# Kernel optimization log

Measured on AMD Instinct MI355X. Metric: run time of the kernel, lower is better.

The kernel has to match this reference:

```python
import jax, jax.numpy as jnp
import numpy as np

B, L, D, FF = 4, 4096, 1024, 2048
EPS = 1e-5


def _ln(x, g, b):
    m = jnp.mean(x, axis=-1, keepdims=True)
    v = jnp.var(x, axis=-1, keepdims=True)
    return (x - m) / jnp.sqrt(v + EPS) * g + b


def setup_inputs() -> dict:
    key = jax.random.key(0)
    ks = jax.random.split(key, 9)
    x = jax.random.normal(ks[0], (B, L, D), jnp.float32)
    # phazor init: exp(2j*pi*k/D) * |randn| -> split into re/im float params
    mag = jnp.abs(jax.random.normal(ks[1], (D,), jnp.float32))
    ang = 2.0 * jnp.pi * jnp.arange(D, dtype=jnp.float32) / D
    return dict(
        x=x,
        ln_g=jnp.ones((D,), jnp.float32),
        ln_b=jnp.zeros((D,), jnp.float32),
        fc_w=jax.random.normal(ks[2], (D, D), jnp.float32) * 0.02,
        fc_b=jnp.zeros((D,), jnp.float32),
        w1=jax.random.normal(ks[3], (D, FF), jnp.float32) * 0.02,
        b1=jnp.zeros((FF,), jnp.float32),
        w2=jax.random.normal(ks[4], (FF, D), jnp.float32) * 0.02,
        b2=jnp.zeros((D,), jnp.float32),
        ph_re=mag * jnp.cos(ang),
        ph_im=mag * jnp.sin(ang),
        phi_re=jax.random.normal(ks[5], (D,), jnp.float32),
        phi_im=jax.random.normal(ks[6], (D,), jnp.float32),
        lci_re=jax.random.normal(ks[7], (D,), jnp.float32),
        lci_im=jax.random.normal(ks[8], (D,), jnp.float32),
    )


def _spiral_conv(xn, ph_re, ph_im, phi_re, phi_im, lci_re, lci_im):
    ph = ph_re + 1j * ph_im          # phazor parameter [D]
    phi = phi_re + 1j * phi_im       # phazor_init [D]
    lci = lci_re + 1j * lci_im       # last_conv_init [D]
    a = jnp.abs(ph)
    phz = ph / a * jnp.exp(-a)       # unit direction * decaying magnitude, [D]
    t = jnp.arange(L, dtype=jnp.float32)[:, None]
    prog = jnp.exp(t * jnp.log(phz)[None, :])        # phz**t, [L, D]
    filt = prog * phi[None, :]                       # [L, D]
    filt_fft = jnp.fft.fft(filt, n=2 * L, axis=0)    # [2L, D]
    x_fft = jnp.fft.fft(xn.astype(jnp.complex64), n=2 * L, axis=1)  # [B, 2L, D]
    conv = jnp.fft.ifft(filt_fft[None] * x_fft, axis=1)[:, :L]      # [B, L, D]
    # last_conv is detached in the original (first call uses last_conv_init)
    last = jax.lax.stop_gradient(lci)
    conv = conv + last[None, None, :] * prog[None] * phz[None, None, :]
    return conv.real


def reference(x, ln_g, ln_b, fc_w, fc_b, w1, b1, w2, b2,
              ph_re, ph_im, phi_re, phi_im, lci_re, lci_im):
    xn = _ln(x, ln_g, ln_b)
    c = _spiral_conv(xn, ph_re, ph_im, phi_re, phi_im, lci_re, lci_im)
    y = jax.nn.silu(x @ fc_w + fc_b)
    x2 = c * y + x                  # gated conv + residual (dropout=0 -> identity)
    x3 = _ln(x2, ln_g, ln_b)        # same (shared) LayerNorm instance
    h = jax.nn.silu(x3 @ w1 + b1) @ w2 + b2
    return x2 + h
```

## Files before the change

kernel.cpp:

```cpp
#include <hip/hip_runtime.h>
#include <hip/hip_bf16.h>
#include <hip/hip_fp8.h>
#include <cstdint>
#include <cstddef>

#define B_ 4
#define L_ 4096
#define D_ 1024
#define FF_ 2048
#define ROWS (B_ * L_)
#define EPS_ 1e-5f
#define CG 64
#define CC 64

typedef __attribute__((ext_vector_type(8))) __bf16 bf16x8;
typedef __attribute__((ext_vector_type(4))) float f32x4;
typedef __attribute__((ext_vector_type(4))) unsigned short us4;
typedef __attribute__((ext_vector_type(2))) long l2;

__device__ __forceinline__ float bf2f(unsigned short u) {
  union { unsigned int i; float f; } v; v.i = ((unsigned int)u) << 16; return v.f;
}
__device__ __forceinline__ unsigned short f2bf(float f) {
  union { float f; unsigned int i; } v; v.f = f;
  unsigned int r = v.i + 0x7fffu + ((v.i >> 16) & 1u);
  return (unsigned short)(r >> 16);
}
__device__ __forceinline__ unsigned char f2fp8(float f) {
  __hip_fp8_e4m3 q(f);
  return *reinterpret_cast<unsigned char*>(&q);
}
__device__ __forceinline__ int ph64(int e) {
  return (((e >> 3) & 3) << 4) | (((e >> 5) & 1) << 3) | (e & 7);
}

__global__ __launch_bounds__(256) void transpose_cast(
    const float* __restrict__ in, unsigned short* __restrict__ out, int K, int N) {
  __shared__ float tb[32][33];
  int n0 = blockIdx.x * 32, k0 = blockIdx.y * 32;
  int tx = threadIdx.x & 31, ty = threadIdx.x >> 5;
#pragma unroll
  for (int i = 0; i < 4; ++i) {
    int k = ty + i * 8;
    tb[k][tx] = in[(size_t)(k0 + k) * N + n0 + tx];
  }
  __syncthreads();
#pragma unroll
  for (int i = 0; i < 4; ++i) {
    int n = ty + i * 8;
    out[(size_t)(n0 + n) * K + k0 + tx] = f2bf(tb[tx][n]);
  }
}

__global__ __launch_bounds__(256) void transpose_cast_fp8(
    const float* __restrict__ in, unsigned char* __restrict__ out, int K, int N,
    float scale) {
  __shared__ float tb[32][33];
  int n0 = blockIdx.x * 32, k0 = blockIdx.y * 32;
  int tx = threadIdx.x & 31, ty = threadIdx.x >> 5;
#pragma unroll
  for (int i = 0; i < 4; ++i) {
    int k = ty + i * 8;
    tb[k][tx] = in[(size_t)(k0 + k) * N + n0 + tx];
  }
  __syncthreads();
#pragma unroll
  for (int i = 0; i < 4; ++i) {
    int n = ty + i * 8;
    int k = k0 + tx;
    size_t idx = (size_t)(n0 + n) * K + (k & ~63) + ph64(k & 63);
    out[idx] = f2fp8(tb[tx][n] * scale);
  }
}

__global__ __launch_bounds__(256) void ln1_kernel(
    const float* __restrict__ x, const float* __restrict__ g, const float* __restrict__ b,
    unsigned short* __restrict__ xn, unsigned short* __restrict__ xb) {
  int row = blockIdx.x;
  int t = threadIdx.x;
  const float4* xr = (const float4*)(x + (size_t)row * D_);
  float4 v = xr[t];
  float s = v.x + v.y + v.z + v.w;
  float sq = v.x * v.x + v.y * v.y + v.z * v.z + v.w * v.w;
#pragma unroll
  for (int off = 32; off > 0; off >>= 1) {
    s += __shfl_down(s, off);
    sq += __shfl_down(sq, off);
  }
  __shared__ float ls[4], lq[4];
  int lane = t & 63, w = t >> 6;
  if (lane == 0) { ls[w] = s; lq[w] = sq; }
  __syncthreads();
  s = ls[0] + ls[1] + ls[2] + ls[3];
  sq = lq[0] + lq[1] + lq[2] + lq[3];
  float mean = s * (1.0f / D_);
  float var = sq * (1.0f / D_) - mean * mean;
  float rstd = rsqrtf(var + EPS_);
  float4 gv = ((const float4*)g)[t];
  float4 bv = ((const float4*)b)[t];
  us4 o, ob;
  o.x = f2bf((v.x - mean) * rstd * gv.x + bv.x);
  o.y = f2bf((v.y - mean) * rstd * gv.y + bv.y);
  o.z = f2bf((v.z - mean) * rstd * gv.z + bv.z);
  o.w = f2bf((v.w - mean) * rstd * gv.w + bv.w);
  ob.x = f2bf(v.x); ob.y = f2bf(v.y); ob.z = f2bf(v.z); ob.w = f2bf(v.w);
  ((us4*)(xn + (size_t)row * D_))[t] = o;
  ((us4*)(xb + (size_t)row * D_))[t] = ob;
}

__global__ __launch_bounds__(256) void conv_pass1(
    const unsigned short* __restrict__ xn, const float* __restrict__ ph_re,
    const float* __restrict__ ph_im, float2* __restrict__ rloc) {
  int d = blockIdx.x * 256 + threadIdx.x;
  int g = blockIdx.y, b = blockIdx.z;
  float re = ph_re[d], im = ph_im[d];
  float a = sqrtf(re * re + im * im);
  float sc = expf(-a) / a;
  float pr = re * sc, pi = im * sc;
  float rr = 0.f, ri = 0.f;
  const unsigned short* xp = xn + ((size_t)(b * L_ + g * CC)) * D_ + d;
#pragma unroll 8
  for (int l = 0; l < CC; ++l) {
    float xv = bf2f(xp[(size_t)l * D_]);
    float nr = pr * rr - pi * ri + xv;
    ri = pr * ri + pi * rr;
    rr = nr;
  }
  rloc[((size_t)(b * CG + g)) * D_ + d] = make_float2(rr, ri);
}

__global__ __launch_bounds__(256) void conv_pass2(
    const float* __restrict__ ph_re, const float* __restrict__ ph_im,
    const float2* __restrict__ rloc, float2* __restrict__ carry) {
  int idx = blockIdx.x * 256 + threadIdx.x;
  int b = idx >> 10, d = idx & (D_ - 1);
  float re = ph_re[d], im = ph_im[d];
  float a = sqrtf(re * re + im * im);
  float th = atan2f(im, re);
  float rho = expf(-a * (float)CC);
  float ang = th * (float)CC;
  float pcr = rho * cosf(ang), pci = rho * sinf(ang);
  float cr = 0.f, ci = 0.f;
  for (int g0 = 0; g0 < CG; g0 += 8) {
    float2 rl[8];
    float2 cw[8];
#pragma unroll
    for (int i = 0; i < 8; ++i)
      rl[i] = rloc[((size_t)(b * CG + g0 + i)) * D_ + d];
#pragma unroll
    for (int i = 0; i < 8; ++i) {
      cw[i] = make_float2(cr, ci);
      float nr = pcr * cr - pci * ci + rl[i].x;
      ci = pcr * ci + pci * cr + rl[i].y;
      cr = nr;
    }
#pragma unroll
    for (int i = 0; i < 8; ++i)
      carry[((size_t)(b * CG + g0 + i)) * D_ + d] = cw[i];
  }
}

__global__ __launch_bounds__(256) void conv_pass3(
    const unsigned short* __restrict__ xn,
    const float* __restrict__ ph_re, const float* __restrict__ ph_im,
    const float* __restrict__ phi_re, const float* __restrict__ phi_im,
    const float* __restrict__ lci_re, const float* __restrict__ lci_im,
    const float2* __restrict__ carry, unsigned short* __restrict__ cout) {
  int d = blockIdx.x * 256 + threadIdx.x;
  int g = blockIdx.y, b = blockIdx.z;
  float re = ph_re[d], im = ph_im[d];
  float a = sqrtf(re * re + im * im);
  float sc = expf(-a) / a;
  float pr = re * sc, pi = im * sc;
  float th = atan2f(im, re);
  int l0 = g * CC;
  float rho = expf(-a * (float)(l0 + 1));
  float ang = th * (float)(l0 + 1);
  float prr = rho * cosf(ang), pri = rho * sinf(ang);
  float fr = phi_re[d], fi = phi_im[d];
  float qr = lci_re[d], qi = lci_im[d];
  float2 cv = carry[((size_t)(b * CG + g)) * D_ + d];
  float rr = cv.x, ri = cv.y;
  const unsigned short* xp = xn + ((size_t)(b * L_ + l0)) * D_ + d;
  unsigned short* cp = cout + ((size_t)(b * L_ + l0)) * D_ + d;
#pragma unroll 4
  for (int l = 0; l < CC; ++l) {
    float xv = bf2f(xp[(size_t)l * D_]);
    float nr = pr * rr - pi * ri + xv;
    ri = pr * ri + pi * rr;
    rr = nr;
    float outv = fr * rr - fi * ri + qr * prr - qi * pri;
    cp[(size_t)l * D_] = f2bf(outv);
    float pn = pr * prr - pi * pri;
    pri = pr * pri + pi * prr;
    prr = pn;
  }
}

__global__ __launch_bounds__(256) void ln2c_kernel(
    const unsigned short* __restrict__ x2, const float* __restrict__ g,
    const float* __restrict__ b, unsigned char* __restrict__ x3) {
  int row = blockIdx.x;
  int t = threadIdx.x;
  size_t base = (size_t)row * D_;
  us4 vb = ((const us4*)(x2 + base))[t];
  float4 v;
  v.x = bf2f(vb.x); v.y = bf2f(vb.y); v.z = bf2f(vb.z); v.w = bf2f(vb.w);
  float s = v.x + v.y + v.z + v.w;
  float sq = v.x * v.x + v.y * v.y + v.z * v.z + v.w * v.w;
#pragma unroll
  for (int off = 32; off > 0; off >>= 1) {
    s += __shfl_down(s, off);
    sq += __shfl_down(sq, off);
  }
  __shared__ float ls[4], lq[4];
  int lane = t & 63, w = t >> 6;
  if (lane == 0) { ls[w] = s; lq[w] = sq; }
  __syncthreads();
  s = ls[0] + ls[1] + ls[2] + ls[3];
  sq = lq[0] + lq[1] + lq[2] + lq[3];
  float mean = s * (1.0f / D_);
  float var = sq * (1.0f / D_) - mean * mean;
  float rstd = rsqrtf(var + EPS_);
  float4 gv = ((const float4*)g)[t];
  float4 bv = ((const float4*)b)[t];
  uchar4 o;
  o.x = f2fp8((v.x - mean) * rstd * gv.x + bv.x);
  o.y = f2fp8((v.y - mean) * rstd * gv.y + bv.y);
  o.z = f2fp8((v.z - mean) * rstd * gv.z + bv.z);
  o.w = f2fp8((v.w - mean) * rstd * gv.w + bv.w);
  int d = t * 4;
  size_t idx = base + (size_t)((d & ~63) + ph64(d & 63));
  *((uchar4*)(x3 + idx)) = o;
}

__device__ __forceinline__ void gld_lds16(const void* gp, void* lp) {
  __builtin_amdgcn_global_load_lds(
      (const __attribute__((address_space(1))) unsigned int*)gp,
      (__attribute__((address_space(3))) unsigned int*)lp, 16, 0, 0);
}

__global__ __launch_bounds__(512) void gemm_bt_gate(
    const unsigned short* __restrict__ A, const unsigned short* __restrict__ Bt,
    const float* __restrict__ bias,
    const unsigned short* __restrict__ gate, const float* __restrict__ xresf,
    unsigned short* __restrict__ Cv, int NB, int GROUP, int N, int K) {
  __shared__ unsigned short As[3][256 * 64];
  __shared__ unsigned short Bs[3][128 * 64];

  int nwg = gridDim.x;
  int xcd = blockIdx.x & 7;
  int lo = blockIdx.x >> 3;
  int q = nwg >> 3;
  int gsz = GROUP * NB;
  int g_ = lo / gsz, r_ = lo % gsz;
  int n_ = r_ / GROUP, ml = r_ - n_ * GROUP;
  int Mx = q / NB;
  int bm0 = (xcd * Mx + g_ * GROUP + ml) * 256;
  int bn0 = n_ * 128;

  int t = threadIdx.x;
  int lane = t & 63, w = t >> 6;
  int wr = w >> 1, wc = w & 1;
  int frr = lane & 15, cl = lane >> 4;
  int fx = frr & 7;
  int rA0 = wr * 64 + frr;
  int rB0 = wc * 64 + frr;
  int ko0 = (cl ^ fx) * 8;
  int ko1 = ((4 + cl) ^ fx) * 8;

  int nt = K >> 6;

  int tr = t >> 3;
  int jx = (t & 7) ^ (tr & 7);
  const unsigned short* pA = A + (size_t)(bm0 + tr) * K + jx * 8;
  const unsigned short* pB = Bt + (size_t)(bn0 + tr) * K + jx * 8;

  auto stA = [&](int kt2, int slot, int c) {
    gld_lds16(pA + (size_t)kt2 * 64 + (size_t)c * 64 * K, &As[slot][c * 4096 + t * 8]);
  };
  auto stB = [&](int kt2, int slot, int c) {
    gld_lds16(pB + (size_t)kt2 * 64 + (size_t)c * 64 * K, &Bs[slot][c * 4096 + t * 8]);
  };

  f32x4 acc[4][4] = {};

  stA(0, 0, 0); stA(0, 0, 1); stA(0, 0, 2); stA(0, 0, 3); stB(0, 0, 0); stB(0, 0, 1);
  stA(1, 1, 0); stA(1, 1, 1); stA(1, 1, 2); stA(1, 1, 3); stB(1, 1, 0); stB(1, 1, 1);
  asm volatile("s_waitcnt vmcnt(6)" ::: "memory");
  __builtin_amdgcn_s_barrier();

  int s = 0;
  for (int kt = 0; kt < nt; ++kt) {
    const unsigned short* as = As[s];
    const unsigned short* bs = Bs[s];
    int s2 = s + 2; if (s2 >= 3) s2 -= 3;
    bool p2 = kt + 2 < nt;

    bf16x8 a0[4], b0[4], a1[4], b1[4];
#pragma unroll
    for (int m = 0; m < 4; ++m) a0[m] = *(const bf16x8*)&as[(rA0 + m * 16) * 64 + ko0];
#pragma unroll
    for (int n = 0; n < 4; ++n) b0[n] = *(const bf16x8*)&bs[(rB0 + n * 16) * 64 + ko0];
#pragma unroll
    for (int m = 0; m < 4; ++m) a1[m] = *(const bf16x8*)&as[(rA0 + m * 16) * 64 + ko1];
#pragma unroll
    for (int n = 0; n < 4; ++n) b1[n] = *(const bf16x8*)&bs[(rB0 + n * 16) * 64 + ko1];
    if (p2) {
      stA(kt + 2, s2, 0); stA(kt + 2, s2, 1); stA(kt + 2, s2, 2); stA(kt + 2, s2, 3);
      stB(kt + 2, s2, 0); stB(kt + 2, s2, 1);
    }

    asm volatile("s_waitcnt lgkmcnt(0)" ::: "memory");
    __builtin_amdgcn_sched_barrier(0);
    __builtin_amdgcn_s_setprio(1);
#pragma unroll
    for (int m = 0; m < 4; ++m)
#pragma unroll
      for (int n = 0; n < 4; ++n)
        acc[m][n] = __builtin_amdgcn_mfma_f32_16x16x32_bf16(a0[m], b0[n], acc[m][n], 0, 0, 0);
#pragma unroll
    for (int m = 0; m < 4; ++m)
#pragma unroll
      for (int n = 0; n < 4; ++n)
        acc[m][n] = __builtin_amdgcn_mfma_f32_16x16x32_bf16(a1[m], b1[n], acc[m][n], 0, 0, 0);
    __builtin_amdgcn_s_setprio(0);

    if (p2) { asm volatile("s_waitcnt vmcnt(6)" ::: "memory"); }
    else    { asm volatile("s_waitcnt vmcnt(0)" ::: "memory"); }
    __builtin_amdgcn_s_barrier();
    s += 1; if (s == 3) s = 0;
  }

#pragma unroll
  for (int m = 0; m < 4; ++m) {
#pragma unroll
    for (int n = 0; n < 4; ++n) {
#pragma unroll
      for (int r = 0; r < 4; ++r) {
        int row = bm0 + wr * 64 + m * 16 + cl * 4 + r;
        int col = bn0 + wc * 64 + n * 16 + frr;
        size_t o = (size_t)row * N + col;
        float v = acc[m][n][r] + bias[col];
        v = v / (1.0f + __expf(-v));
        v = bf2f(gate[o]) * v + xresf[o];
        Cv[o] = f2bf(v);
      }
    }
  }
}

template <int SILU, int RESBF, int OUT_FP8>
__global__ __launch_bounds__(512, 4) void gemm_f8(
    const unsigned char* __restrict__ A, const unsigned char* __restrict__ Bt,
    const float* __restrict__ bias, const unsigned short* __restrict__ resb,
    float oscale, void* __restrict__ Cv, int NB, int GROUP, int N, int K) {
  __shared__ unsigned char As[3][256 * 64];
  __shared__ unsigned char Bs[3][128 * 64];

  int nwg = gridDim.x;
  int xcd = blockIdx.x & 7;
  int lo = blockIdx.x >> 3;
  int q = nwg >> 3;
  int gsz = GROUP * NB;
  int g_ = lo / gsz, r_ = lo % gsz;
  int n_ = r_ / GROUP, ml = r_ - n_ * GROUP;
  int Mx = q / NB;
  int bm0 = (xcd * Mx + g_ * GROUP + ml) * 256;
  int bn0 = n_ * 128;

  int t = threadIdx.x;
  int lane = t & 63, w = t >> 6;
  int wr = w >> 1, wc = w & 1;
  int frr = lane & 15, cl = lane >> 4;
  int sw = (frr >> 1) & 3;
  int rA0 = wr * 64 + frr;
  int rB0 = wc * 64 + frr;
  int ko = (cl ^ sw) * 16;

  int nt = K >> 6;

  int tr = t >> 2;
  int jc = (t & 3) ^ ((tr >> 1) & 3);
  const unsigned char* pA = A + (size_t)(bm0 + tr) * K + jc * 16;
  const unsigned char* pB = Bt + (size_t)(bn0 + tr) * K + jc * 16;

  auto stA = [&](int kt2, int slot, int c) {
    gld_lds16(pA + (size_t)kt2 * 64 + (size_t)c * 128 * K, &As[slot][c * 8192 + t * 16]);
  };
  auto stB = [&](int kt2, int slot) {
    gld_lds16(pB + (size_t)kt2 * 64, &Bs[slot][t * 16]);
  };

  f32x4 acc[4][4] = {};

  stA(0, 0, 0); stA(0, 0, 1); stB(0, 0);
  stA(1, 1, 0); stA(1, 1, 1); stB(1, 1);
  asm volatile("s_waitcnt vmcnt(3)" ::: "memory");
  __builtin_amdgcn_s_barrier();

  int s = 0;
  for (int kt = 0; kt < nt; ++kt) {
    const unsigned char* as = As[s];
    const unsigned char* bs = Bs[s];
    int s2 = s + 2; if (s2 >= 3) s2 -= 3;
    bool p2 = kt + 2 < nt;

    l2 av[4], bv[4];
#pragma unroll
    for (int m = 0; m < 4; ++m) av[m] = *(const l2*)&as[(rA0 + m * 16) * 64 + ko];
#pragma unroll
    for (int n = 0; n < 4; ++n) bv[n] = *(const l2*)&bs[(rB0 + n * 16) * 64 + ko];
    if (p2) { stA(kt + 2, s2, 0); stA(kt + 2, s2, 1); stB(kt + 2, s2); }

    asm volatile("s_waitcnt lgkmcnt(0)" ::: "memory");
    __builtin_amdgcn_sched_barrier(0);
    __builtin_amdgcn_s_setprio(1);
#pragma unroll
    for (int m = 0; m < 4; ++m)
#pragma unroll
      for (int n = 0; n < 4; ++n)
        acc[m][n] = __builtin_amdgcn_mfma_f32_16x16x32_fp8_fp8(av[m].x, bv[n].x, acc[m][n], 0, 0, 0);
#pragma unroll
    for (int m = 0; m < 4; ++m)
#pragma unroll
      for (int n = 0; n < 4; ++n)
        acc[m][n] = __builtin_amdgcn_mfma_f32_16x16x32_fp8_fp8(av[m].y, bv[n].y, acc[m][n], 0, 0, 0);
    __builtin_amdgcn_s_setprio(0);

    if (p2) { asm volatile("s_waitcnt vmcnt(3)" ::: "memory"); }
    else    { asm volatile("s_waitcnt vmcnt(0)" ::: "memory"); }
    __builtin_amdgcn_s_barrier();
    s += 1; if (s == 3) s = 0;
  }

#pragma unroll
  for (int m = 0; m < 4; ++m) {
#pragma unroll
    for (int n = 0; n < 4; ++n) {
#pragma unroll
      for (int r = 0; r < 4; ++r) {
        int row = bm0 + wr * 64 + m * 16 + cl * 4 + r;
        int col = bn0 + wc * 64 + n * 16 + frr;
        size_t o = (size_t)row * N + col;
        float v = acc[m][n][r] * oscale + bias[col];
        if (SILU) v = v / (1.0f + __expf(-v));
        if (RESBF) v += bf2f(resb[o]);
        if (OUT_FP8) {
          int e = n * 16 + frr;
          size_t op = (size_t)row * N + bn0 + wc * 64 + ph64(e);
          ((unsigned char*)Cv)[op] = f2fp8(v);
        } else {
          ((float*)Cv)[o] = v;
        }
      }
    }
  }
}

extern "C" void kernel_launch(void* const* d_in, const int* in_sizes, int n_in,
                              void* d_out, int out_size, void* d_ws, size_t ws_size,
                              hipStream_t stream) {
  const float* x      = (const float*)d_in[0];
  const float* ln_g   = (const float*)d_in[1];
  const float* ln_b   = (const float*)d_in[2];
  const float* fc_w   = (const float*)d_in[3];
  const float* fc_b   = (const float*)d_in[4];
  const float* w1     = (const float*)d_in[5];
  const float* b1     = (const float*)d_in[6];
  const float* w2     = (const float*)d_in[7];
  const float* b2     = (const float*)d_in[8];
  const float* ph_re  = (const float*)d_in[9];
  const float* ph_im  = (const float*)d_in[10];
  const float* phi_re = (const float*)d_in[11];
  const float* phi_im = (const float*)d_in[12];
  const float* lci_re = (const float*)d_in[13];
  const float* lci_im = (const float*)d_in[14];
  float* out = (float*)d_out;

  char* ws = (char*)d_ws;
  const size_t SZ_BF = (size_t)ROWS * D_ * 2;
  const size_t SZ_F8 = (size_t)ROWS * D_;
  unsigned short* xn_x2 = (unsigned short*)(ws);
  unsigned short* cbuf  = (unsigned short*)(ws + SZ_BF);
  unsigned short* xb    = (unsigned short*)(ws + 2 * SZ_BF);
  unsigned char*  x3f8  = (unsigned char*)(ws + 3 * SZ_BF);
  unsigned char*  h1f8  = (unsigned char*)(ws + 3 * SZ_BF + SZ_F8);
  char* wp = ws + 3 * SZ_BF + SZ_F8 + (size_t)ROWS * FF_;
  unsigned short* fc_wt = (unsigned short*)(wp);
  unsigned char*  w1t8  = (unsigned char*)(wp + (size_t)D_ * D_ * 2);
  unsigned char*  w2t8  = (unsigned char*)(wp + (size_t)D_ * D_ * 2 + (size_t)D_ * FF_);
  float2* rloc  = (float2*)(wp + (size_t)D_ * D_ * 2 + 2 * (size_t)D_ * FF_);
  float2* carry = rloc + (size_t)B_ * CG * D_;

  transpose_cast<<<dim3(D_ / 32, D_ / 32), 256, 0, stream>>>(fc_w, fc_wt, D_, D_);
  transpose_cast_fp8<<<dim3(FF_ / 32, D_ / 32), 256, 0, stream>>>(w1, w1t8, D_, FF_, 32.0f);
  transpose_cast_fp8<<<dim3(D_ / 32, FF_ / 32), 256, 0, stream>>>(w2, w2t8, FF_, D_, 32.0f);

  ln1_kernel<<<ROWS, 256, 0, stream>>>(x, ln_g, ln_b, xn_x2, xb);

  conv_pass1<<<dim3(D_ / 256, CG, B_), 256, 0, stream>>>(xn_x2, ph_re, ph_im, rloc);
  conv_pass2<<<dim3((B_ * D_) / 256), 256, 0, stream>>>(ph_re, ph_im, rloc, carry);
  conv_pass3<<<dim3(D_ / 256, CG, B_), 256, 0, stream>>>(xn_x2, ph_re, ph_im, phi_re, phi_im,
                                                         lci_re, lci_im, carry, cbuf);

  gemm_bt_gate<<<(ROWS / 256) * (D_ / 128), 512, 0, stream>>>(
      xb, fc_wt, fc_b, cbuf, x, xn_x2, D_ / 128, 4, D_, D_);

  ln2c_kernel<<<ROWS, 256, 0, stream>>>(xn_x2, ln_g, ln_b, x3f8);

  gemm_f8<1, 0, 1><<<(ROWS / 256) * (FF_ / 128), 512, 0, stream>>>(
      x3f8, w1t8, b1, nullptr, 1.0f / 32.0f, h1f8, FF_ / 128, 4, FF_, D_);

  gemm_f8<0, 1, 0><<<(ROWS / 256) * (D_ / 128), 512, 0, stream>>>(
      h1f8, w2t8, b2, xn_x2, 1.0f / 32.0f, out, D_ / 128, 2, D_, FF_);
}
```

Measured before the change: 259.6 us.

## Halve K-tile in gate GEMM for higher occupancy and read bf16 residual

The gated fc GEMM now uses a 32-wide K tile instead of 64, which halves LDS use (about 72KB to 36KB) and drops half the fragment registers, with launch bounds requesting 4 waves per SIMD. The swizzle and load mapping are reworked to match. The residual is now read from the bf16 copy of x instead of the fp32 original, which cuts epilogue memory traffic but adds rounding error to the residual term. Each iteration now does half the MFMA work per barrier, so sync overhead per FLOP doubles.

```diff
diff --git a/kernel.cpp b/kernel.cpp
--- a/kernel.cpp
+++ b/kernel.cpp
@@ -240,13 +240,13 @@
       (__attribute__((address_space(3))) unsigned int*)lp, 16, 0, 0);
 }
 
-__global__ __launch_bounds__(512) void gemm_bt_gate(
+__global__ __launch_bounds__(512, 4) void gemm_bt_gate(
     const unsigned short* __restrict__ A, const unsigned short* __restrict__ Bt,
     const float* __restrict__ bias,
-    const unsigned short* __restrict__ gate, const float* __restrict__ xresf,
+    const unsigned short* __restrict__ gate, const unsigned short* __restrict__ xresb,
     unsigned short* __restrict__ Cv, int NB, int GROUP, int N, int K) {
-  __shared__ unsigned short As[3][256 * 64];
-  __shared__ unsigned short Bs[3][128 * 64];
+  __shared__ unsigned short As[3][256 * 32];
+  __shared__ unsigned short Bs[3][128 * 32];
 
   int nwg = gridDim.x;
   int xcd = blockIdx.x & 7;
@@ -263,31 +263,30 @@
   int lane = t & 63, w = t >> 6;
   int wr = w >> 1, wc = w & 1;
   int frr = lane & 15, cl = lane >> 4;
-  int fx = frr & 7;
+  int sw = (frr >> 1) & 3;
   int rA0 = wr * 64 + frr;
   int rB0 = wc * 64 + frr;
-  int ko0 = (cl ^ fx) * 8;
-  int ko1 = ((4 + cl) ^ fx) * 8;
-
-  int nt = K >> 6;
-
-  int tr = t >> 3;
-  int jx = (t & 7) ^ (tr & 7);
-  const unsigned short* pA = A + (size_t)(bm0 + tr) * K + jx * 8;
-  const unsigned short* pB = Bt + (size_t)(bn0 + tr) * K + jx * 8;
+  int ko = (cl ^ sw) * 8;
+
+  int nt = K >> 5;
+
+  int tr = t >> 2;
+  int jc = (t & 3) ^ ((tr >> 1) & 3);
+  const unsigned short* pA = A + (size_t)(bm0 + tr) * K + jc * 8;
+  const unsigned short* pB = Bt + (size_t)(bn0 + tr) * K + jc * 8;
 
   auto stA = [&](int kt2, int slot, int c) {
-    gld_lds16(pA + (size_t)kt2 * 64 + (size_t)c * 64 * K, &As[slot][c * 4096 + t * 8]);
+    gld_lds16(pA + (size_t)kt2 * 32 + (size_t)c * 128 * K, &As[slot][c * 4096 + t * 8]);
   };
-  auto stB = [&](int kt2, int slot, int c) {
-    gld_lds16(pB + (size_t)kt2 * 64 + (size_t)c * 64 * K, &Bs[slot][c * 4096 + t * 8]);
+  auto stB = [&](int kt2, int slot) {
+    gld_lds16(pB + (size_t)kt2 * 32, &Bs[slot][t * 8]);
   };
 
   f32x4 acc[4][4] = {};
 
-  stA(0, 0, 0); stA(0, 0, 1); stA(0, 0, 2); stA(0, 0, 3); stB(0, 0, 0); stB(0, 0, 1);
-  stA(1, 1, 0); stA(1, 1, 1); stA(1, 1, 2); stA(1, 1, 3); stB(1, 1, 0); stB(1, 1, 1);
-  asm volatile("s_waitcnt vmcnt(6)" ::: "memory");
+  stA(0, 0, 0); stA(0, 0, 1); stB(0, 0);
+  stA(1, 1, 0); stA(1, 1, 1); stB(1, 1);
+  asm volatile("s_waitcnt vmcnt(3)" ::: "memory");
   __builtin_amdgcn_s_barrier();
 
   int s = 0;
@@ -297,19 +296,12 @@
     int s2 = s + 2; if (s2 >= 3) s2 -= 3;
     bool p2 = kt + 2 < nt;
 
-    bf16x8 a0[4], b0[4], a1[4], b1[4];
-#pragma unroll
-    for (int m = 0; m < 4; ++m) a0[m] = *(const bf16x8*)&as[(rA0 + m * 16) * 64 + ko0];
-#pragma unroll
-    for (int n = 0; n < 4; ++n) b0[n] = *(const bf16x8*)&bs[(rB0 + n * 16) * 64 + ko0];
-#pragma unroll
-    for (int m = 0; m < 4; ++m) a1[m] = *(const bf16x8*)&as[(rA0 + m * 16) * 64 + ko1];
-#pragma unroll
-    for (int n = 0; n < 4; ++n) b1[n] = *(const bf16x8*)&bs[(rB0 + n * 16) * 64 + ko1];
-    if (p2) {
-      stA(kt + 2, s2, 0); stA(kt + 2, s2, 1); stA(kt + 2, s2, 2); stA(kt + 2, s2, 3);
-      stB(kt + 2, s2, 0); stB(kt + 2, s2, 1);
-    }
+    bf16x8 av[4], bv[4];
+#pragma unroll
+    for (int m = 0; m < 4; ++m) av[m] = *(const bf16x8*)&as[(rA0 + m * 16) * 32 + ko];
+#pragma unroll
+    for (int n = 0; n < 4; ++n) bv[n] = *(const bf16x8*)&bs[(rB0 + n * 16) * 32 + ko];
+    if (p2) { stA(kt + 2, s2, 0); stA(kt + 2, s2, 1); stB(kt + 2, s2); }
 
     asm volatile("s_waitcnt lgkmcnt(0)" ::: "memory");
     __builtin_amdgcn_sched_barrier(0);
@@ -318,15 +310,10 @@
     for (int m = 0; m < 4; ++m)
 #pragma unroll
       for (int n = 0; n < 4; ++n)
-        acc[m][n] = __builtin_amdgcn_mfma_f32_16x16x32_bf16(a0[m], b0[n], acc[m][n], 0, 0, 0);
-#pragma unroll
-    for (int m = 0; m < 4; ++m)
-#pragma unroll
-      for (int n = 0; n < 4; ++n)
-        acc[m][n] = __builtin_amdgcn_mfma_f32_16x16x32_bf16(a1[m], b1[n], acc[m][n], 0, 0, 0);
+        acc[m][n] = __builtin_amdgcn_mfma_f32_16x16x32_bf16(av[m], bv[n], acc[m][n], 0, 0, 0);
     __builtin_amdgcn_s_setprio(0);
 
-    if (p2) { asm volatile("s_waitcnt vmcnt(6)" ::: "memory"); }
+    if (p2) { asm volatile("s_waitcnt vmcnt(3)" ::: "memory"); }
     else    { asm volatile("s_waitcnt vmcnt(0)" ::: "memory"); }
     __builtin_amdgcn_s_barrier();
     s += 1; if (s == 3) s = 0;
@@ -343,7 +330,7 @@
         size_t o = (size_t)row * N + col;
         float v = acc[m][n][r] + bias[col];
         v = v / (1.0f + __expf(-v));
-        v = bf2f(gate[o]) * v + xresf[o];
+        v = bf2f(gate[o]) * v + bf2f(xresb[o]);
         Cv[o] = f2bf(v);
       }
     }
@@ -505,7 +492,7 @@
                                                          lci_re, lci_im, carry, cbuf);
 
   gemm_bt_gate<<<(ROWS / 256) * (D_ / 128), 512, 0, stream>>>(
-      xb, fc_wt, fc_b, cbuf, x, xn_x2, D_ / 128, 4, D_, D_);
+      xb, fc_wt, fc_b, cbuf, xb, xn_x2, D_ / 128, 4, D_, D_);
 
   ln2c_kernel<<<ROWS, 256, 0, stream>>>(xn_x2, ln_g, ln_b, x3f8);
 
```

Result: faster. 247.9 us (-4.5%).
